# Kernel optimization log

Hardware: AMD Instinct MI355X
Metric: run time of the kernel (lower is better)

## Reference

```python
import jax, jax.numpy as jnp
import numpy as np

B, F, E, A, T, H = 16384, 1024, 28, 2, 128, 4
HD = T // H  # head dim = 32

def _ln(x, g, b, eps=1e-5):
    m = jnp.mean(x, axis=-1, keepdims=True)
    v = jnp.var(x, axis=-1, keepdims=True)
    return (x - m) / jnp.sqrt(v + eps) * g + b

def _gelu(x):
    return jax.nn.gelu(x, approximate=False)  # torch nn.GELU default (erf)

def setup_inputs() -> dict:
    key = jax.random.key(0)
    ks = iter(jax.random.split(key, 48))
    def rn(shape, s=0.02):
        return jax.random.normal(next(ks), shape, jnp.float32) * s
    d = dict(
        fusion_feat=jax.random.normal(next(ks), (B, F), jnp.float32),
        explicit_logits=jax.random.normal(next(ks), (B, E), jnp.float32),
        implicit_logits=jax.random.normal(next(ks), (B, E), jnp.float32),
        affect_vec=jax.random.normal(next(ks), (B, A), jnp.float32),
        ln_exp_g=jnp.ones((E,), jnp.float32), ln_exp_b=jnp.zeros((E,), jnp.float32),
        W_exp=rn((E, T)), b_exp=jnp.zeros((T,), jnp.float32),
        ln_imp_g=jnp.ones((E,), jnp.float32), ln_imp_b=jnp.zeros((E,), jnp.float32),
        W_imp=rn((E, T)), b_imp=jnp.zeros((T,), jnp.float32),
        ln_aff_g=jnp.ones((A,), jnp.float32), ln_aff_b=jnp.zeros((A,), jnp.float32),
        W_aff=rn((A, T)), b_aff=jnp.zeros((T,), jnp.float32),
        Wq_in=rn((F, T)), bq_in=jnp.zeros((T,), jnp.float32),   # query_proj
        Wq=rn((T, T)), bq=jnp.zeros((T,), jnp.float32),         # MHA in_proj q
        Wk=rn((T, T)), bk=jnp.zeros((T,), jnp.float32),         # MHA in_proj k
        Wv=rn((T, T)), bv=jnp.zeros((T,), jnp.float32),         # MHA in_proj v
        Wo=rn((T, T)), bo=jnp.zeros((T,), jnp.float32),         # MHA out_proj
        Wc=rn((T, F)), bc=jnp.zeros((F,), jnp.float32),         # context_proj
        Ws=rn((3 * T, F)), bs=jnp.zeros((F,), jnp.float32),     # summary_proj
        Wg1=rn((2 * F, F)), bg1=jnp.zeros((F,), jnp.float32),   # gate layer 1
        Wg2=rn((F, F)), bg2=jnp.zeros((F,), jnp.float32),       # gate layer 2
        ln_out_g=jnp.ones((F,), jnp.float32), ln_out_b=jnp.zeros((F,), jnp.float32),
    )
    return d

def reference(fusion_feat, explicit_logits, implicit_logits, affect_vec,
              ln_exp_g, ln_exp_b, W_exp, b_exp,
              ln_imp_g, ln_imp_b, W_imp, b_imp,
              ln_aff_g, ln_aff_b, W_aff, b_aff,
              Wq_in, bq_in, Wq, bq, Wk, bk, Wv, bv, Wo, bo,
              Wc, bc, Ws, bs, Wg1, bg1, Wg2, bg2, ln_out_g, ln_out_b):
    p_exp = jax.nn.softmax(explicit_logits, axis=-1)
    p_imp = jax.nn.softmax(implicit_logits, axis=-1)
    exp_e = _gelu(_ln(p_exp, ln_exp_g, ln_exp_b) @ W_exp + b_exp)       # (B,T)
    imp_e = _gelu(_ln(p_imp, ln_imp_g, ln_imp_b) @ W_imp + b_imp)       # (B,T)
    aff_e = _gelu(_ln(affect_vec, ln_aff_g, ln_aff_b) @ W_aff + b_aff)  # (B,T)
    tokens = jnp.stack([exp_e, imp_e, aff_e], axis=1)                   # (B,3,T)
    q = fusion_feat @ Wq_in + bq_in                                     # (B,T)
    # tiny 1-query x 3-key multi-head cross attention (dropout=eval/identity)
    qh = (q @ Wq + bq).reshape(B, H, HD)
    kh = (tokens @ Wk + bk).reshape(B, 3, H, HD)
    vh = (tokens @ Wv + bv).reshape(B, 3, H, HD)
    scores = jnp.einsum('bhd,bshd->bhs', qh, kh) / np.float32(np.sqrt(HD))
    w = jax.nn.softmax(scores, axis=-1)                                 # (B,H,3)
    attn_weights = jnp.mean(w, axis=1)                                  # avg heads -> (B,3)
    attn_out = jnp.einsum('bhs,bshd->bhd', w, vh).reshape(B, T) @ Wo + bo
    context = attn_out @ Wc + bc                                        # (B,F)
    gate_h = _gelu(jnp.concatenate([fusion_feat, context], axis=-1) @ Wg1 + bg1)
    gate = jax.nn.sigmoid(gate_h @ Wg2 + bg2)
    refined = _ln(fusion_feat + gate * context, ln_out_g, ln_out_b)
    summary = _gelu(jnp.concatenate([exp_e, imp_e, aff_e], axis=-1) @ Ws + bs)
    return refined, attn_weights, summary
```

## Files before the change

### kernel.cpp

```cpp
#include <hip/hip_runtime.h>
#include <hip/hip_bf16.h>
#include <stdint.h>


using bf16 = __hip_bfloat16;
typedef __bf16 bf16x8 __attribute__((ext_vector_type(8)));
typedef float f32x4 __attribute__((ext_vector_type(4)));

__device__ __forceinline__ float b2f(bf16 x) { return __bfloat162float(x); }
__device__ __forceinline__ bf16 f2b(float x) { return __float2bfloat16(x); }
__device__ __forceinline__ float gelu_f(float x) {
  return 0.5f * x * (1.0f + erff(x * 0.70710678118654752f));
}

__device__ __forceinline__ void async_ld16(const void* g, void* l) {
  using GP = const __attribute__((address_space(1))) uint32_t*;
  using LP = __attribute__((address_space(3))) uint32_t*;
  __builtin_amdgcn_global_load_lds((GP)g, (LP)l, 16, 0, 0);
}

__global__ void ffb_convert(const float* __restrict__ src, bf16* __restrict__ dst) {
  size_t i = ((size_t)blockIdx.x * 256 + threadIdx.x) * 4;
  float4 v = *reinterpret_cast<const float4*>(src + i);
  ushort4 o;
  o.x = __builtin_bit_cast(unsigned short, f2b(v.x));
  o.y = __builtin_bit_cast(unsigned short, f2b(v.y));
  o.z = __builtin_bit_cast(unsigned short, f2b(v.z));
  o.w = __builtin_bit_cast(unsigned short, f2b(v.w));
  *reinterpret_cast<ushort4*>(dst + i) = o;
}

template <int EPI, typename OutT>
__launch_bounds__(256)
__global__ void gemm128(const bf16* A0, const bf16* A1, int ksplit, int lda0, int lda1,
                        const bf16* __restrict__ BT, int K,
                        const float* __restrict__ bias,
                        OutT* out, int ldo,
                        const float* ffp, const bf16* ctxp, int ldfc)
{
  __shared__ uint16_t smA[128 * 64];
  __shared__ uint16_t smB[128 * 64];
  const int tid = threadIdx.x;
  const int w = tid >> 6;
  const int l = tid & 63;
  const int m0 = blockIdx.x * 128;
  const int n0 = blockIdx.y * 128;
  const int wr = w >> 1, wc = w & 1;
  const int lrow = l & 15, lquad = l >> 4;
  const int rb = w * 8 + (l >> 3);
  const int cpos = l & 7;

  const f32x4 vzero = {0.f, 0.f, 0.f, 0.f};
  f32x4 acc[4][4];
#pragma unroll
  for (int i = 0; i < 4; i++)
#pragma unroll
    for (int j = 0; j < 4; j++) acc[i][j] = vzero;

  for (int k0 = 0; k0 < K; k0 += 64) {
    __syncthreads();
#pragma unroll
    for (int i = 0; i < 4; i++) {
      int row = i * 32 + rb;
      int cg = cpos ^ (row & 7);
      int kcol = k0 + cg * 8;
      const bf16* gp = (kcol < ksplit)
                           ? (A0 + (size_t)(m0 + row) * lda0 + kcol)
                           : (A1 + (size_t)(m0 + row) * lda1 + (kcol - ksplit));
      async_ld16(gp, &smA[(i * 32 + w * 8) * 64]);
      const bf16* gq = BT + (size_t)(n0 + row) * K + k0 + cg * 8;
      async_ld16(gq, &smB[(i * 32 + w * 8) * 64]);
    }
    __syncthreads();
#pragma unroll
    for (int kk = 0; kk < 2; kk++) {
      bf16x8 af[4], bfr[4];
      const int cc = kk * 4 + lquad;
#pragma unroll
      for (int mi = 0; mi < 4; mi++) {
        int r = wr * 64 + mi * 16 + lrow;
        af[mi] = *(const bf16x8*)&smA[r * 64 + ((cc ^ (r & 7)) << 3)];
      }
#pragma unroll
      for (int ni = 0; ni < 4; ni++) {
        int r = wc * 64 + ni * 16 + lrow;
        bfr[ni] = *(const bf16x8*)&smB[r * 64 + ((cc ^ (r & 7)) << 3)];
      }
#pragma unroll
      for (int mi = 0; mi < 4; mi++)
#pragma unroll
        for (int ni = 0; ni < 4; ni++)
          acc[mi][ni] =
              __builtin_amdgcn_mfma_f32_16x16x32_bf16(af[mi], bfr[ni], acc[mi][ni], 0, 0, 0);
    }
  }

#pragma unroll
  for (int mi = 0; mi < 4; mi++) {
#pragma unroll
    for (int ni = 0; ni < 4; ni++) {
#pragma unroll
      for (int r = 0; r < 4; r++) {
        int row = m0 + wr * 64 + mi * 16 + lquad * 4 + r;
        int col = n0 + wc * 64 + ni * 16 + lrow;
        float v = acc[mi][ni][r] + bias[col];
        if (EPI == 1) v = gelu_f(v);
        if (EPI == 2) {
          float gate = 1.f / (1.f + expf(-v));
          size_t fo = (size_t)row * ldfc + col;
          v = ffp[fo] + gate * b2f(ctxp[fo]);
        }
        if constexpr (__is_same(OutT, float))
          out[(size_t)row * ldo + col] = v;
        else
          out[(size_t)row * ldo + col] = f2b(v);
      }
    }
  }
}

__global__ void prep_kernel(
    const float* __restrict__ Wq_in, const float* __restrict__ bq_in,
    const float* __restrict__ Wq, const float* __restrict__ bq,
    const float* __restrict__ Wk, const float* __restrict__ bk,
    const float* __restrict__ Wv, const float* __restrict__ bv,
    const float* __restrict__ Wo, const float* __restrict__ bo,
    const float* __restrict__ Wc, const float* __restrict__ bc,
    const float* __restrict__ Ws, const float* __restrict__ Wg1,
    const float* __restrict__ Wg2,
    bf16* WKVT, float* BKV, bf16* WQQT, float* BQQ, bf16* WOCT, float* BOC,
    bf16* WST, bf16* WG1T, bf16* WG2T)
{
  int idx = blockIdx.x * 256 + threadIdx.x;
  if (idx < 32768) {
    int n = idx >> 7, k = idx & 127;
    WKVT[idx] = f2b((n < 128) ? Wk[k * 128 + n] : Wv[k * 128 + (n - 128)]);
    return;
  }
  idx -= 32768;
  if (idx < 256) { BKV[idx] = (idx < 128) ? bk[idx] : bv[idx - 128]; return; }
  idx -= 256;
  if (idx < 131072) {
    int t = idx >> 10, f = idx & 1023;
    float s = 0.f;
    for (int u = 0; u < 128; u++) s += Wq_in[f * 128 + u] * Wq[u * 128 + t];
    WQQT[idx] = f2b(s);
    return;
  }
  idx -= 131072;
  if (idx < 128) {
    float s = bq[idx];
    for (int u = 0; u < 128; u++) s += bq_in[u] * Wq[u * 128 + idx];
    BQQ[idx] = s;
    return;
  }
  idx -= 128;
  if (idx < 131072) {
    int f = idx >> 7, d = idx & 127;
    float s = 0.f;
    for (int t = 0; t < 128; t++) s += Wo[d * 128 + t] * Wc[t * 1024 + f];
    WOCT[idx] = f2b(s);
    return;
  }
  idx -= 131072;
  if (idx < 1024) {
    float s = bc[idx];
    for (int t = 0; t < 128; t++) s += bo[t] * Wc[t * 1024 + idx];
    BOC[idx] = s;
    return;
  }
  idx -= 1024;
  if (idx < 393216) { int f = idx / 384, j = idx % 384; WST[idx] = f2b(Ws[j * 1024 + f]); return; }
  idx -= 393216;
  if (idx < 2097152) { int f = idx >> 11, j = idx & 2047; WG1T[idx] = f2b(Wg1[j * 1024 + f]); return; }
  idx -= 2097152;
  if (idx < 1048576) { int f = idx >> 10, j = idx & 1023; WG2T[idx] = f2b(Wg2[j * 1024 + f]); return; }
}

__device__ __forceinline__ void emb28(const float* __restrict__ logits,
                                      const float* __restrict__ g,
                                      const float* __restrict__ bb,
                                      const float* __restrict__ W,
                                      const float* __restrict__ wb,
                                      bf16* __restrict__ out, int t,
                                      float* sv, float* sp)
{
  if (t < 28) sv[t] = logits[t];
  __syncthreads();
  float mx = sv[0];
#pragma unroll
  for (int e = 1; e < 28; e++) mx = fmaxf(mx, sv[e]);
  if (t < 28) sp[t] = expf(sv[t] - mx);
  __syncthreads();
  float sum = 0.f;
#pragma unroll
  for (int e = 0; e < 28; e++) sum += sp[e];
  float inv = 1.f / sum;
  float sp2 = 0.f;
#pragma unroll
  for (int e = 0; e < 28; e++) { float p = sp[e] * inv; sp2 += p * p; }
  const float mean = 1.f / 28.f;
  float var = sp2 * (1.f / 28.f) - mean * mean;
  float rstd = rsqrtf(var + 1e-5f);
  __syncthreads();
  if (t < 28) sp[t] = (sp[t] * inv - mean) * rstd * g[t] + bb[t];
  __syncthreads();
  float acc = wb[t];
#pragma unroll
  for (int e = 0; e < 28; e++) acc += sp[e] * W[e * 128 + t];
  out[t] = f2b(gelu_f(acc));
  __syncthreads();
}

__global__ void tokens_kernel(
    const float* __restrict__ exl, const float* __restrict__ iml, const float* __restrict__ affv,
    const float* __restrict__ geg, const float* __restrict__ geb,
    const float* __restrict__ Wex, const float* __restrict__ bex,
    const float* __restrict__ gig, const float* __restrict__ gib,
    const float* __restrict__ Wim, const float* __restrict__ bim,
    const float* __restrict__ gag, const float* __restrict__ gab,
    const float* __restrict__ Waf, const float* __restrict__ baf,
    bf16* __restrict__ tokens)
{
  __shared__ float sv[28], sp[28];
  const int b = blockIdx.x, t = threadIdx.x;
  bf16* trow = tokens + (size_t)b * 384;
  emb28(exl + (size_t)b * 28, geg, geb, Wex, bex, trow, t, sv, sp);
  emb28(iml + (size_t)b * 28, gig, gib, Wim, bim, trow + 128, t, sv, sp);
  float a0 = affv[(size_t)b * 2 + 0];
  float a1 = affv[(size_t)b * 2 + 1];
  float m = 0.5f * (a0 + a1);
  float d0 = a0 - m, d1 = a1 - m;
  float var = 0.5f * (d0 * d0 + d1 * d1);
  float rstd = rsqrtf(var + 1e-5f);
  float l0 = d0 * rstd * gag[0] + gab[0];
  float l1 = d1 * rstd * gag[1] + gab[1];
  float acc = baf[t] + l0 * Waf[t] + l1 * Waf[128 + t];
  trow[256 + t] = f2b(gelu_f(acc));
}

__global__ void attn_kernel(const bf16* __restrict__ qh, const bf16* __restrict__ kvh,
                            bf16* __restrict__ apre, float* __restrict__ attw)
{
  const int b = blockIdx.x, t = threadIdx.x;
  float q = b2f(qh[(size_t)b * 128 + t]);
  const bf16* kv = kvh + (size_t)b * 3 * 256;
  float s[3], v[3];
#pragma unroll
  for (int i = 0; i < 3; i++) {
    float k = b2f(kv[i * 256 + t]);
    v[i] = b2f(kv[i * 256 + 128 + t]);
    float r = q * k;
#pragma unroll
    for (int off = 16; off > 0; off >>= 1) r += __shfl_down(r, off, 32);
    r = __shfl(r, 0, 32);
    s[i] = r * 0.17677669529663687f;
  }
  float mx = fmaxf(s[0], fmaxf(s[1], s[2]));
  float e0 = expf(s[0] - mx), e1 = expf(s[1] - mx), e2 = expf(s[2] - mx);
  float inv = 1.f / (e0 + e1 + e2);
  float w0 = e0 * inv, w1 = e1 * inv, w2 = e2 * inv;
  apre[(size_t)b * 128 + t] = f2b(w0 * v[0] + w1 * v[1] + w2 * v[2]);
  __shared__ float aw[4][3];
  if ((t & 31) == 0) { int h = t >> 5; aw[h][0] = w0; aw[h][1] = w1; aw[h][2] = w2; }
  __syncthreads();
  if (t < 3)
    attw[(size_t)b * 3 + t] = 0.25f * (aw[0][t] + aw[1][t] + aw[2][t] + aw[3][t]);
}

__global__ void ln_out_kernel(const bf16* __restrict__ x, const float* __restrict__ g,
                              const float* __restrict__ bb, float* __restrict__ out)
{
  const int row = blockIdx.x, t = threadIdx.x;
  const bf16* xr = x + (size_t)row * 1024;
  ushort4 u = *reinterpret_cast<const ushort4*>(xr + t * 4);
  float v0 = __uint_as_float((uint32_t)u.x << 16);
  float v1 = __uint_as_float((uint32_t)u.y << 16);
  float v2 = __uint_as_float((uint32_t)u.z << 16);
  float v3 = __uint_as_float((uint32_t)u.w << 16);
  float s = v0 + v1 + v2 + v3;
  float s2 = v0 * v0 + v1 * v1 + v2 * v2 + v3 * v3;
#pragma unroll
  for (int off = 32; off > 0; off >>= 1) {
    s += __shfl_down(s, off, 64);
    s2 += __shfl_down(s2, off, 64);
  }
  __shared__ float ls[4], ls2[4];
  const int w = t >> 6;
  if ((t & 63) == 0) { ls[w] = s; ls2[w] = s2; }
  __syncthreads();
  float S = ls[0] + ls[1] + ls[2] + ls[3];
  float S2 = ls2[0] + ls2[1] + ls2[2] + ls2[3];
  float mean = S * (1.f / 1024.f);
  float var = S2 * (1.f / 1024.f) - mean * mean;
  float rstd = rsqrtf(var + 1e-5f);
  const int c = t * 4;
  float4 o;
  o.x = (v0 - mean) * rstd * g[c + 0] + bb[c + 0];
  o.y = (v1 - mean) * rstd * g[c + 1] + bb[c + 1];
  o.z = (v2 - mean) * rstd * g[c + 2] + bb[c + 2];
  o.w = (v3 - mean) * rstd * g[c + 3] + bb[c + 3];
  *reinterpret_cast<float4*>(out + (size_t)row * 1024 + c) = o;
}

extern "C" void kernel_launch(void* const* d_in, const int* in_sizes, int n_in,
                              void* d_out, int out_size, void* d_ws, size_t ws_size,
                              hipStream_t stream)
{
  const float* ff   = (const float*)d_in[0];
  const float* exl  = (const float*)d_in[1];
  const float* iml  = (const float*)d_in[2];
  const float* affv = (const float*)d_in[3];
  const float* geg = (const float*)d_in[4],  *geb = (const float*)d_in[5];
  const float* Wex = (const float*)d_in[6],  *bex = (const float*)d_in[7];
  const float* gig = (const float*)d_in[8],  *gib = (const float*)d_in[9];
  const float* Wim = (const float*)d_in[10], *bim = (const float*)d_in[11];
  const float* gag = (const float*)d_in[12], *gab = (const float*)d_in[13];
  const float* Waf = (const float*)d_in[14], *baf = (const float*)d_in[15];
  const float* Wq_in = (const float*)d_in[16], *bq_in = (const float*)d_in[17];
  const float* Wq = (const float*)d_in[18], *bq = (const float*)d_in[19];
  const float* Wk = (const float*)d_in[20], *bk = (const float*)d_in[21];
  const float* Wv = (const float*)d_in[22], *bv = (const float*)d_in[23];
  const float* Wo = (const float*)d_in[24], *bo = (const float*)d_in[25];
  const float* Wc = (const float*)d_in[26], *bc = (const float*)d_in[27];
  const float* Ws = (const float*)d_in[28], *bs = (const float*)d_in[29];
  const float* Wg1 = (const float*)d_in[30], *bg1 = (const float*)d_in[31];
  const float* Wg2 = (const float*)d_in[32], *bg2 = (const float*)d_in[33];
  const float* lng = (const float*)d_in[34], *lnb = (const float*)d_in[35];

  char* ws = (char*)d_ws;
  bf16*  WKVT = (bf16*)(ws + 0);
  float* BKV  = (float*)(ws + 65536);
  bf16*  WQQT = (bf16*)(ws + 66560);
  float* BQQ  = (float*)(ws + 328704);
  bf16*  WOCT = (bf16*)(ws + 329216);
  float* BOC  = (float*)(ws + 591360);
  bf16*  WST  = (bf16*)(ws + 595456);
  bf16*  WG1T = (bf16*)(ws + 1381888);
  bf16*  WG2T = (bf16*)(ws + 5576192);
  bf16*  FFB  = (bf16*)(ws + 7673344);
  bf16*  PRE  = (bf16*)(ws + 7673344);
  bf16*  TOK  = (bf16*)(ws + 41227776);
  bf16*  QH   = (bf16*)(ws + 53810688);
  bf16*  APRE = (bf16*)(ws + 58004992);

  float* outp = (float*)d_out;
  float* out_refined = outp;
  float* out_attw    = outp + 16777216;
  float* out_summary = outp + 16826368;
  bf16* CTX   = (bf16*)out_refined;
  bf16* KVH   = (bf16*)out_summary;
  bf16* GATEH = (bf16*)out_summary;

  ffb_convert<<<16384, 256, 0, stream>>>(ff, FFB);
  prep_kernel<<<14982, 256, 0, stream>>>(Wq_in, bq_in, Wq, bq, Wk, bk, Wv, bv,
                                         Wo, bo, Wc, bc, Ws, Wg1, Wg2,
                                         WKVT, BKV, WQQT, BQQ, WOCT, BOC,
                                         WST, WG1T, WG2T);
  tokens_kernel<<<16384, 128, 0, stream>>>(exl, iml, affv, geg, geb, Wex, bex,
                                           gig, gib, Wim, bim, gag, gab, Waf, baf, TOK);
  gemm128<0, bf16><<<dim3(128, 1), 256, 0, stream>>>(FFB, FFB, 1024, 1024, 1024, WQQT, 1024,
                                                     BQQ, QH, 128, nullptr, nullptr, 0);
  gemm128<0, bf16><<<dim3(384, 2), 256, 0, stream>>>(TOK, TOK, 128, 128, 128, WKVT, 128,
                                                     BKV, KVH, 256, nullptr, nullptr, 0);
  attn_kernel<<<16384, 128, 0, stream>>>(QH, KVH, APRE, out_attw);
  gemm128<0, bf16><<<dim3(128, 8), 256, 0, stream>>>(APRE, APRE, 128, 128, 128, WOCT, 128,
                                                     BOC, CTX, 1024, nullptr, nullptr, 0);
  gemm128<1, bf16><<<dim3(128, 8), 256, 0, stream>>>(FFB, CTX, 1024, 1024, 1024, WG1T, 2048,
                                                     bg1, GATEH, 1024, nullptr, nullptr, 0);
  gemm128<2, bf16><<<dim3(128, 8), 256, 0, stream>>>(GATEH, GATEH, 1024, 1024, 1024, WG2T, 1024,
                                                     bg2, PRE, 1024, ff, CTX, 1024);
  gemm128<1, float><<<dim3(128, 8), 256, 0, stream>>>(TOK, TOK, 384, 384, 384, WST, 384,
                                                      bs, out_summary, 1024, nullptr, nullptr, 0);
  ln_out_kernel<<<16384, 256, 0, stream>>>(PRE, lng, lnb, out_refined);
}
```

Before: 593.9 us.

## Template GEMM M-tile, use fast tanh GELU/expf, read bf16 residual in gate epilogue

```diff
diff --git a/kernel.cpp b/kernel.cpp
--- a/kernel.cpp
+++ b/kernel.cpp
@@ -9,8 +9,18 @@
 
 __device__ __forceinline__ float b2f(bf16 x) { return __bfloat162float(x); }
 __device__ __forceinline__ bf16 f2b(float x) { return __float2bfloat16(x); }
+
+__device__ __forceinline__ float fast_tanh(float y) {
+  float z = fabsf(y);
+  float t = __expf(-2.f * z);
+  float r = (1.f - t) / (1.f + t);
+  return copysignf(r, y);
+}
 __device__ __forceinline__ float gelu_f(float x) {
-  return 0.5f * x * (1.0f + erff(x * 0.70710678118654752f));
+  return 0.5f * x * (1.f + fast_tanh(0.7978845608028654f * (x + 0.044715f * x * x * x)));
+}
+__device__ __forceinline__ float sigmoid_f(float v) {
+  return 1.f / (1.f + __expf(-v));
 }
 
 __device__ __forceinline__ void async_ld16(const void* g, void* l) {
@@ -30,20 +40,21 @@
   *reinterpret_cast<ushort4*>(dst + i) = o;
 }
 
-template <int EPI, typename OutT>
+template <int EPI, typename OutT, int MT>
 __launch_bounds__(256)
 __global__ void gemm128(const bf16* A0, const bf16* A1, int ksplit, int lda0, int lda1,
                         const bf16* __restrict__ BT, int K,
                         const float* __restrict__ bias,
                         OutT* out, int ldo,
-                        const float* ffp, const bf16* ctxp, int ldfc)
-{
-  __shared__ uint16_t smA[128 * 64];
+                        const bf16* ffp, const bf16* ctxp, int ldfc)
+{
+  constexpr int MIC = MT / 32;
+  __shared__ uint16_t smA[MT * 64];
   __shared__ uint16_t smB[128 * 64];
   const int tid = threadIdx.x;
   const int w = tid >> 6;
   const int l = tid & 63;
-  const int m0 = blockIdx.x * 128;
+  const int m0 = blockIdx.x * MT;
   const int n0 = blockIdx.y * 128;
   const int wr = w >> 1, wc = w & 1;
   const int lrow = l & 15, lquad = l >> 4;
@@ -51,16 +62,16 @@
   const int cpos = l & 7;
 
   const f32x4 vzero = {0.f, 0.f, 0.f, 0.f};
-  f32x4 acc[4][4];
-#pragma unroll
-  for (int i = 0; i < 4; i++)
+  f32x4 acc[MIC][4];
+#pragma unroll
+  for (int i = 0; i < MIC; i++)
 #pragma unroll
     for (int j = 0; j < 4; j++) acc[i][j] = vzero;
 
   for (int k0 = 0; k0 < K; k0 += 64) {
     __syncthreads();
 #pragma unroll
-    for (int i = 0; i < 4; i++) {
+    for (int i = 0; i < MIC; i++) {
       int row = i * 32 + rb;
       int cg = cpos ^ (row & 7);
       int kcol = k0 + cg * 8;
@@ -68,17 +79,22 @@
                            ? (A0 + (size_t)(m0 + row) * lda0 + kcol)
                            : (A1 + (size_t)(m0 + row) * lda1 + (kcol - ksplit));
       async_ld16(gp, &smA[(i * 32 + w * 8) * 64]);
+    }
+#pragma unroll
+    for (int i = 0; i < 4; i++) {
+      int row = i * 32 + rb;
+      int cg = cpos ^ (row & 7);
       const bf16* gq = BT + (size_t)(n0 + row) * K + k0 + cg * 8;
       async_ld16(gq, &smB[(i * 32 + w * 8) * 64]);
     }
     __syncthreads();
 #pragma unroll
     for (int kk = 0; kk < 2; kk++) {
-      bf16x8 af[4], bfr[4];
+      bf16x8 af[MIC], bfr[4];
       const int cc = kk * 4 + lquad;
 #pragma unroll
-      for (int mi = 0; mi < 4; mi++) {
-        int r = wr * 64 + mi * 16 + lrow;
+      for (int mi = 0; mi < MIC; mi++) {
+        int r = wr * (MT / 2) + mi * 16 + lrow;
         af[mi] = *(const bf16x8*)&smA[r * 64 + ((cc ^ (r & 7)) << 3)];
       }
 #pragma unroll
@@ -87,7 +103,7 @@
         bfr[ni] = *(const bf16x8*)&smB[r * 64 + ((cc ^ (r & 7)) << 3)];
       }
 #pragma unroll
-      for (int mi = 0; mi < 4; mi++)
+      for (int mi = 0; mi < MIC; mi++)
 #pragma unroll
         for (int ni = 0; ni < 4; ni++)
           acc[mi][ni] =
@@ -96,19 +112,19 @@
   }
 
 #pragma unroll
-  for (int mi = 0; mi < 4; mi++) {
+  for (int mi = 0; mi < MIC; mi++) {
 #pragma unroll
     for (int ni = 0; ni < 4; ni++) {
 #pragma unroll
       for (int r = 0; r < 4; r++) {
-        int row = m0 + wr * 64 + mi * 16 + lquad * 4 + r;
+        int row = m0 + wr * (MT / 2) + mi * 16 + lquad * 4 + r;
         int col = n0 + wc * 64 + ni * 16 + lrow;
         float v = acc[mi][ni][r] + bias[col];
         if (EPI == 1) v = gelu_f(v);
         if (EPI == 2) {
-          float gate = 1.f / (1.f + expf(-v));
+          float gate = sigmoid_f(v);
           size_t fo = (size_t)row * ldfc + col;
-          v = ffp[fo] + gate * b2f(ctxp[fo]);
+          v = b2f(ffp[fo]) + gate * b2f(ctxp[fo]);
         }
         if constexpr (__is_same(OutT, float))
           out[(size_t)row * ldo + col] = v;
@@ -190,7 +206,7 @@
   float mx = sv[0];
 #pragma unroll
   for (int e = 1; e < 28; e++) mx = fmaxf(mx, sv[e]);
-  if (t < 28) sp[t] = expf(sv[t] - mx);
+  if (t < 28) sp[t] = __expf(sv[t] - mx);
   __syncthreads();
   float sum = 0.f;
 #pragma unroll
@@ -257,7 +273,7 @@
     s[i] = r * 0.17677669529663687f;
   }
   float mx = fmaxf(s[0], fmaxf(s[1], s[2]));
-  float e0 = expf(s[0] - mx), e1 = expf(s[1] - mx), e2 = expf(s[2] - mx);
+  float e0 = __expf(s[0] - mx), e1 = __expf(s[1] - mx), e2 = __expf(s[2] - mx);
   float inv = 1.f / (e0 + e1 + e2);
   float w0 = e0 * inv, w1 = e1 * inv, w2 = e2 * inv;
   apre[(size_t)b * 128 + t] = f2b(w0 * v[0] + w1 * v[1] + w2 * v[2]);
@@ -359,18 +375,18 @@
                                          WST, WG1T, WG2T);
   tokens_kernel<<<16384, 128, 0, stream>>>(exl, iml, affv, geg, geb, Wex, bex,
                                            gig, gib, Wim, bim, gag, gab, Waf, baf, TOK);
-  gemm128<0, bf16><<<dim3(128, 1), 256, 0, stream>>>(FFB, FFB, 1024, 1024, 1024, WQQT, 1024,
-                                                     BQQ, QH, 128, nullptr, nullptr, 0);
-  gemm128<0, bf16><<<dim3(384, 2), 256, 0, stream>>>(TOK, TOK, 128, 128, 128, WKVT, 128,
-                                                     BKV, KVH, 256, nullptr, nullptr, 0);
+  gemm128<0, bf16, 64><<<dim3(256, 1), 256, 0, stream>>>(FFB, FFB, 1024, 1024, 1024, WQQT, 1024,
+                                                         BQQ, QH, 128, nullptr, nullptr, 0);
+  gemm128<0, bf16, 128><<<dim3(384, 2), 256, 0, stream>>>(TOK, TOK, 128, 128, 128, WKVT, 128,
+                                                          BKV, KVH, 256, nullptr, nullptr, 0);
   attn_kernel<<<16384, 128, 0, stream>>>(QH, KVH, APRE, out_attw);
-  gemm128<0, bf16><<<dim3(128, 8), 256, 0, stream>>>(APRE, APRE, 128, 128, 128, WOCT, 128,
-                                                     BOC, CTX, 1024, nullptr, nullptr, 0);
-  gemm128<1, bf16><<<dim3(128, 8), 256, 0, stream>>>(FFB, CTX, 1024, 1024, 1024, WG1T, 2048,
-                                                     bg1, GATEH, 1024, nullptr, nullptr, 0);
-  gemm128<2, bf16><<<dim3(128, 8), 256, 0, stream>>>(GATEH, GATEH, 1024, 1024, 1024, WG2T, 1024,
-                                                     bg2, PRE, 1024, ff, CTX, 1024);
-  gemm128<1, float><<<dim3(128, 8), 256, 0, stream>>>(TOK, TOK, 384, 384, 384, WST, 384,
-                                                      bs, out_summary, 1024, nullptr, nullptr, 0);
+  gemm128<0, bf16, 128><<<dim3(128, 8), 256, 0, stream>>>(APRE, APRE, 128, 128, 128, WOCT, 128,
+                                                          BOC, CTX, 1024, nullptr, nullptr, 0);
+  gemm128<1, bf16, 128><<<dim3(128, 8), 256, 0, stream>>>(FFB, CTX, 1024, 1024, 1024, WG1T, 2048,
+                                                          bg1, GATEH, 1024, nullptr, nullptr, 0);
+  gemm128<2, bf16, 128><<<dim3(128, 8), 256, 0, stream>>>(GATEH, GATEH, 1024, 1024, 1024, WG2T, 1024,
+                                                          bg2, PRE, 1024, FFB, CTX, 1024);
+  gemm128<1, float, 128><<<dim3(128, 8), 256, 0, stream>>>(TOK, TOK, 384, 384, 384, WST, 384,
+                                                           bs, out_summary, 1024, nullptr, nullptr, 0);
   ln_out_kernel<<<16384, 256, 0, stream>>>(PRE, lng, lnb, out_refined);
 }
```

Result: faster. 557.3 us (-6.2%).
